# Optimization experiments

Measured on AMD Instinct MI355X. Metric: run time of the kernel, lower is better.

## Reference

```python
import jax, jax.numpy as jnp
import numpy as np

IM_SIZE = (256, 256)
OVERSAMP = 1.25
WIDTH = 6
BETA = float(np.pi * np.sqrt((WIDTH / OVERSAMP * (OVERSAMP - 0.5)) ** 2 - 0.8))
OS_SIZE = tuple(int(np.ceil(OVERSAMP * n)) for n in IM_SIZE)  # (320, 320)
D = 2


def _kb(x):
    # Kaiser-Bessel interpolation kernel: i0(beta*sqrt(1-x^2)) for |x|<=1 (sigpy convention)
    return jnp.i0(BETA * jnp.sqrt(jnp.maximum(1.0 - x * x, 0.0)))


def setup_inputs() -> dict:
    key = jax.random.key(0)
    k1, k2, k3 = jax.random.split(key, 3)
    N, C = 1, 8
    img_r = jax.random.normal(k1, (N, C) + IM_SIZE, dtype=jnp.float32)
    img_i = jax.random.normal(k2, (N, C) + IM_SIZE, dtype=jnp.float32)
    # trajectory in [-N_i/2, N_i/2] per the class docstring
    trj = (jax.random.uniform(k3, (N, 64, 4096, D), dtype=jnp.float32) - 0.5) * 256.0
    return {"img_r": img_r, "img_i": img_i, "trj": trj}


def _nufft_forward(img_r, img_i, trj):
    img = (img_r + 1j * img_i).astype(jnp.complex64)  # (N, C, H, W)
    nd = img.ndim
    # --- apodization (inverse FT of KB kernel), separable per axis ---
    for a in range(D):
        n, osn = IM_SIZE[a], OS_SIZE[a]
        idx = jnp.arange(n, dtype=jnp.float32)
        arg = jnp.sqrt(BETA ** 2 - (np.pi * WIDTH * (idx - n // 2) / osn) ** 2)
        apod = arg / jnp.sinh(arg)
        shape = [1] * nd
        shape[nd - D + a] = n
        img = img * apod.reshape(shape)
    # --- scale + centered zero-pad to oversampled grid ---
    img = img / np.sqrt(float(np.prod(IM_SIZE)))
    pads = [(0, 0)] * (nd - D) + [(((o - n) // 2), (o - n) - ((o - n) // 2))
                                  for n, o in zip(IM_SIZE, OS_SIZE)]
    img = jnp.pad(img, pads)
    # --- centered FFT (ifftshift -> fftn(norm=None) -> fftshift) ---
    axes = tuple(range(-D, 0))
    ksp_os = jnp.fft.fftshift(jnp.fft.fftn(jnp.fft.ifftshift(img, axes=axes), axes=axes), axes=axes)
    # --- scale trajectory to oversampled grid coordinates ---
    scale = jnp.array([OS_SIZE[a] / IM_SIZE[a] for a in range(D)], jnp.float32)
    shift = jnp.array([OS_SIZE[a] // 2 for a in range(D)], jnp.float32)
    coord = trj * scale + shift  # (N, R, S, 2)
    x0 = jnp.ceil(coord - WIDTH / 2.0)
    # --- KB interpolation: fixed 6x6 neighbor loop, vectorized gather over all points ---
    N = img.shape[0]
    out = jnp.zeros((N,) + img.shape[1:nd - D] + coord.shape[1:-1], jnp.complex64)

    def gather(grid, ix, iy):  # grid (C, Hos, Wos), ix/iy (R, S) -> (C, R, S)
        return grid[:, ix, iy]

    for dx in range(WIDTH):
        px = x0[..., 0] + dx
        wx = _kb((px - coord[..., 0]) / (WIDTH / 2.0))
        ix = px.astype(jnp.int32) % OS_SIZE[0]
        for dy in range(WIDTH):
            py = x0[..., 1] + dy
            wy = _kb((py - coord[..., 1]) / (WIDTH / 2.0))
            iy = py.astype(jnp.int32) % OS_SIZE[1]
            vals = jax.vmap(gather)(ksp_os, ix, iy)  # (N, C, R, S)
            out = out + vals * (wx * wy)[:, None, :, :]
    return out / (WIDTH ** D)


def reference(img_r, img_i, trj):
    return _nufft_forward(img_r, img_i, trj)
```

## Files before the change

### kernel.cpp

```cpp
#include <hip/hip_runtime.h>
#include <math.h>

#define NCH   8
#define IMN   256
#define OSN   320
#define NPTS  (64*4096)
#define KD    512
#define BETA_F   10.9551078f
#define BETA2_F  120.014389f
#define APOD_C   0.05890486225f

typedef unsigned short u16;
typedef unsigned int   u32;
typedef __attribute__((ext_vector_type(8))) short s16x8;
typedef __attribute__((ext_vector_type(4))) float f32x4;

__device__ __forceinline__ u32 f2bf(float f) {
    u32 u = __float_as_uint(f);
    return (u + 0x7FFFu + ((u >> 16) & 1u)) >> 16;
}

__device__ __forceinline__ float i0f(float t) {
    if (t < 3.75f) {
        float y = t * t * (1.0f / 14.0625f);
        return 1.0f + y * (3.5156229f + y * (3.0899424f + y * (1.2067492f +
                     y * (0.2659732f + y * (0.0360768f + y * 0.0045813f)))));
    }
    float z = 3.75f / t;
    float p = 0.39894228f + z * (0.01328592f + z * (0.00225319f + z * (-0.00157565f +
              z * (0.00916281f + z * (-0.02057706f + z * (0.02635537f +
              z * (-0.01647633f + z * 0.00392377f)))))));
    return expf(t) * rsqrtf(t) * p;
}

__device__ __forceinline__ float apodf(int i) {
    float x = APOD_C * (float)(i - IMN / 2);
    float arg = sqrtf(BETA2_F - x * x);
    float e = expf(arg);
    float sh = 0.5f * (e - 1.0f / e);
    return arg / sh;
}

__global__ void prep_const(u32* __restrict__ B1, u32* __restrict__ B2) {
    int idx = blockIdx.x * 256 + threadIdx.x;
    int k = idx >> 8, j = idx & 255;
    int p = (k * (j + 32)) % OSN;
    float th = (2.0f * (float)M_PI / (float)OSN) * (float)p;
    float s = ((k + j) & 1) ? -1.0f : 1.0f;
    float sn, cs;
    sincosf(th, &sn, &cs);
    float re = s * cs, im = -s * sn;
    B1[idx] = f2bf(re) | (f2bf(-im) << 16);
    B2[idx] = f2bf(im) | (f2bf(re) << 16);
}

__global__ void prep_a(const float* __restrict__ r, const float* __restrict__ im,
                       u32* __restrict__ A) {
    int idx = blockIdx.x * 256 + threadIdx.x;
    int i2 = idx & 255, i1 = (idx >> 8) & 255;
    float w = apodf(i1) * apodf(i2) * (1.0f / 256.0f);
    A[idx] = f2bf(r[idx] * w) | (f2bf(im[idx] * w) << 16);
}

__launch_bounds__(256)
__global__ void gemm1(const short* __restrict__ Abf, const short* __restrict__ B1,
                      const short* __restrict__ B2, short* __restrict__ Tb) {
    const int c = blockIdx.z;
    const int mBase = blockIdx.y * 64;
    const int nBase = blockIdx.x * 64;
    __shared__ short As[64][40], B1s[64][40], B2s[64][40];
    const int t = threadIdx.x;
    const int l = t & 63, w = t >> 6;
    const int wy = w >> 1, wx = w & 1;
    const int row = t >> 2, seg = (t & 3) * 8;
    const int fm = l & 15, fq = (l >> 4) * 8;
    f32x4 zz = {0.f, 0.f, 0.f, 0.f};
    f32x4 accRe[2][2], accIm[2][2];
    #pragma unroll
    for (int i = 0; i < 2; i++)
        #pragma unroll
        for (int j = 0; j < 2; j++) { accRe[i][j] = zz; accIm[i][j] = zz; }

    for (int kc = 0; kc < 16; kc++) {
        const int kb = kc * 32 + seg;
        *(s16x8*)&As [row][seg] = *(const s16x8*)(Abf + ((long)(c * IMN + mBase + row)) * KD + kb);
        *(s16x8*)&B1s[row][seg] = *(const s16x8*)(B1 + (long)(nBase + row) * KD + kb);
        *(s16x8*)&B2s[row][seg] = *(const s16x8*)(B2 + (long)(nBase + row) * KD + kb);
        __syncthreads();
        s16x8 a0  = *(const s16x8*)&As [wy * 32 + fm][fq];
        s16x8 a1  = *(const s16x8*)&As [wy * 32 + 16 + fm][fq];
        s16x8 b10 = *(const s16x8*)&B1s[wx * 32 + fm][fq];
        s16x8 b11 = *(const s16x8*)&B1s[wx * 32 + 16 + fm][fq];
        s16x8 b20 = *(const s16x8*)&B2s[wx * 32 + fm][fq];
        s16x8 b21 = *(const s16x8*)&B2s[wx * 32 + 16 + fm][fq];
        accRe[0][0] = __builtin_amdgcn_mfma_f32_16x16x32_bf16(a0, b10, accRe[0][0], 0, 0, 0);
        accRe[0][1] = __builtin_amdgcn_mfma_f32_16x16x32_bf16(a0, b11, accRe[0][1], 0, 0, 0);
        accRe[1][0] = __builtin_amdgcn_mfma_f32_16x16x32_bf16(a1, b10, accRe[1][0], 0, 0, 0);
        accRe[1][1] = __builtin_amdgcn_mfma_f32_16x16x32_bf16(a1, b11, accRe[1][1], 0, 0, 0);
        accIm[0][0] = __builtin_amdgcn_mfma_f32_16x16x32_bf16(a0, b20, accIm[0][0], 0, 0, 0);
        accIm[0][1] = __builtin_amdgcn_mfma_f32_16x16x32_bf16(a0, b21, accIm[0][1], 0, 0, 0);
        accIm[1][0] = __builtin_amdgcn_mfma_f32_16x16x32_bf16(a1, b20, accIm[1][0], 0, 0, 0);
        accIm[1][1] = __builtin_amdgcn_mfma_f32_16x16x32_bf16(a1, b21, accIm[1][1], 0, 0, 0);
        __syncthreads();
    }
    #pragma unroll
    for (int i = 0; i < 2; i++)
        #pragma unroll
        for (int j = 0; j < 2; j++) {
            int i1b = mBase + wy * 32 + i * 16 + (l >> 4) * 4;
            int k2  = nBase + wx * 32 + j * 16 + fm;
            s16x8 v;
            #pragma unroll
            for (int r = 0; r < 4; r++) {
                v[2 * r]     = (short)f2bf(accRe[i][j][r]);
                v[2 * r + 1] = (short)f2bf(accIm[i][j][r]);
            }
            *(s16x8*)(Tb + ((long)(c * OSN + k2)) * KD + 2 * i1b) = v;
        }
}

__launch_bounds__(256)
__global__ void gemm2(const short* __restrict__ B1, const short* __restrict__ B2,
                      const short* __restrict__ Tb, u32* __restrict__ Gb) {
    const int c = blockIdx.z;
    const int mBase = blockIdx.y * 64;
    const int nBase = blockIdx.x * 64;
    __shared__ short A1s[64][40], A2s[64][40], Bs[64][40];
    const int t = threadIdx.x;
    const int l = t & 63, w = t >> 6;
    const int wy = w >> 1, wx = w & 1;
    const int row = t >> 2, seg = (t & 3) * 8;
    const int fm = l & 15, fq = (l >> 4) * 8;
    f32x4 zz = {0.f, 0.f, 0.f, 0.f};
    f32x4 accRe[2][2], accIm[2][2];
    #pragma unroll
    for (int i = 0; i < 2; i++)
        #pragma unroll
        for (int j = 0; j < 2; j++) { accRe[i][j] = zz; accIm[i][j] = zz; }

    for (int kc = 0; kc < 16; kc++) {
        const int kb = kc * 32 + seg;
        *(s16x8*)&A1s[row][seg] = *(const s16x8*)(B1 + (long)(mBase + row) * KD + kb);
        *(s16x8*)&A2s[row][seg] = *(const s16x8*)(B2 + (long)(mBase + row) * KD + kb);
        *(s16x8*)&Bs [row][seg] = *(const s16x8*)(Tb + ((long)(c * OSN + nBase + row)) * KD + kb);
        __syncthreads();
        s16x8 a10 = *(const s16x8*)&A1s[wy * 32 + fm][fq];
        s16x8 a11 = *(const s16x8*)&A1s[wy * 32 + 16 + fm][fq];
        s16x8 a20 = *(const s16x8*)&A2s[wy * 32 + fm][fq];
        s16x8 a21 = *(const s16x8*)&A2s[wy * 32 + 16 + fm][fq];
        s16x8 b0  = *(const s16x8*)&Bs [wx * 32 + fm][fq];
        s16x8 b1  = *(const s16x8*)&Bs [wx * 32 + 16 + fm][fq];
        accRe[0][0] = __builtin_amdgcn_mfma_f32_16x16x32_bf16(a10, b0, accRe[0][0], 0, 0, 0);
        accRe[0][1] = __builtin_amdgcn_mfma_f32_16x16x32_bf16(a10, b1, accRe[0][1], 0, 0, 0);
        accRe[1][0] = __builtin_amdgcn_mfma_f32_16x16x32_bf16(a11, b0, accRe[1][0], 0, 0, 0);
        accRe[1][1] = __builtin_amdgcn_mfma_f32_16x16x32_bf16(a11, b1, accRe[1][1], 0, 0, 0);
        accIm[0][0] = __builtin_amdgcn_mfma_f32_16x16x32_bf16(a20, b0, accIm[0][0], 0, 0, 0);
        accIm[0][1] = __builtin_amdgcn_mfma_f32_16x16x32_bf16(a20, b1, accIm[0][1], 0, 0, 0);
        accIm[1][0] = __builtin_amdgcn_mfma_f32_16x16x32_bf16(a21, b0, accIm[1][0], 0, 0, 0);
        accIm[1][1] = __builtin_amdgcn_mfma_f32_16x16x32_bf16(a21, b1, accIm[1][1], 0, 0, 0);
        __syncthreads();
    }
    #pragma unroll
    for (int i = 0; i < 2; i++)
        #pragma unroll
        for (int j = 0; j < 2; j++) {
            int k2 = nBase + wx * 32 + j * 16 + fm;
            #pragma unroll
            for (int r = 0; r < 4; r++) {
                int k1 = mBase + wy * 32 + i * 16 + (l >> 4) * 4 + r;
                Gb[((long)k1 * OSN + k2) * NCH + c] =
                    f2bf(accRe[i][j][r]) | (f2bf(accIm[i][j][r]) << 16);
            }
        }
}

__global__ void interp_kernel(const float* __restrict__ trj,
                              const u32* __restrict__ grid,
                              u32* __restrict__ out) {
    const int t = threadIdx.x;
    const int c = t & 7;
    const int pl = t >> 3;
    __shared__ float wxs[32][6], wys[32][6];
    __shared__ int   x0s[32], y0s[32];

    if (t < 32) {
        int pt = blockIdx.x * 32 + t;
        float2 tv = *(const float2*)(trj + pt * 2);
        float cx = __fadd_rn(__fmul_rn(tv.x, 1.25f), 160.0f);
        float cy = __fadd_rn(__fmul_rn(tv.y, 1.25f), 160.0f);
        float x0 = ceilf(__fadd_rn(cx, -3.0f));
        float y0 = ceilf(__fadd_rn(cy, -3.0f));
        x0s[t] = (int)x0;
        y0s[t] = (int)y0;
        #pragma unroll
        for (int d = 0; d < 6; d++) {
            float u = __fdiv_rn(__fsub_rn(x0 + (float)d, cx), 3.0f);
            wxs[t][d] = i0f(BETA_F * sqrtf(fmaxf(1.0f - u * u, 0.0f)));
            float ww = __fdiv_rn(__fsub_rn(y0 + (float)d, cy), 3.0f);
            wys[t][d] = i0f(BETA_F * sqrtf(fmaxf(1.0f - ww * ww, 0.0f)));
        }
    }
    __syncthreads();

    int ix[6], iy[6];
    const int x0i = x0s[pl], y0i = y0s[pl];
    #pragma unroll
    for (int d = 0; d < 6; d++) {
        int vx = x0i + d;
        ix[d] = ((vx % OSN) + OSN) % OSN;
        int vy = y0i + d;
        iy[d] = ((vy % OSN) + OSN) % OSN;
    }

    float accRe = 0.f, accIm = 0.f;
    #pragma unroll
    for (int dx = 0; dx < 6; dx++) {
        long base = (long)ix[dx] * OSN;
        float wxv = wxs[pl][dx];
        #pragma unroll
        for (int dy = 0; dy < 6; dy++) {
            u32 g = grid[(base + iy[dy]) * NCH + c];
            float gre = __uint_as_float(g << 16);
            float gim = __uint_as_float(g & 0xFFFF0000u);
            float ww = wxv * wys[pl][dy];
            accRe += gre * ww;
            accIm += gim * ww;
        }
    }
    accRe *= (1.0f / 36.0f);
    accIm *= (1.0f / 36.0f);

    __shared__ float2 lds[256];
    lds[t] = make_float2(accRe, accIm);
    __syncthreads();
    int c2 = t >> 5, p2 = t & 31;
    float2 v = lds[p2 * 8 + c2];
    out[(long)c2 * NPTS + blockIdx.x * 32 + p2] = f2bf(v.y) | (f2bf(v.x) << 16);
}

extern "C" void kernel_launch(void* const* d_in, const int* in_sizes, int n_in,
                              void* d_out, int out_size, void* d_ws, size_t ws_size,
                              hipStream_t stream) {
    const float* img_r = (const float*)d_in[0];
    const float* img_i = (const float*)d_in[1];
    const float* trj   = (const float*)d_in[2];

    char* ob = (char*)d_out;
    short* Tb  = (short*)(ob);
    u32*  B1u  = (u32*)(ob + 2621440);
    u32*  B2u  = (u32*)(ob + 2949120);
    u32*  Au   = (u32*)(ob + 3276800);
    u32*  Gb   = (u32*)d_ws;

    prep_const<<<(OSN * IMN) / 256, 256, 0, stream>>>(B1u, B2u);
    prep_a<<<(NCH * IMN * IMN) / 256, 256, 0, stream>>>(img_r, img_i, Au);
    gemm1<<<dim3(OSN / 64, IMN / 64, NCH), 256, 0, stream>>>(
        (const short*)Au, (const short*)B1u, (const short*)B2u, Tb);
    gemm2<<<dim3(OSN / 64, OSN / 64, NCH), 256, 0, stream>>>(
        (const short*)B1u, (const short*)B2u, Tb, Gb);
    interp_kernel<<<NPTS / 32, 256, 0, stream>>>(trj, Gb, (u32*)d_out);
}
```

Before: 126.4 us.

## Halve GEMM tile width with 2-wave blocks and widen interp channel loads

Both DFT GEMMs now use 64x32 output tiles with 128-thread blocks, two waves each. This doubles the block count on the small per-channel grids so more CUs stay busy. The interpolation kernel now handles 64 points per block, and each thread loads two channels with one 8-byte load. That halves the gather instruction count and the trajectory/weight setup per point. The cost is lower per-block reuse of the shared B operand in the GEMMs and more register use in the interpolation.

```diff
diff --git a/kernel.cpp b/kernel.cpp
--- a/kernel.cpp
+++ b/kernel.cpp
@@ -62,17 +62,17 @@
     A[idx] = f2bf(r[idx] * w) | (f2bf(im[idx] * w) << 16);
 }
 
-__launch_bounds__(256)
+__launch_bounds__(128)
 __global__ void gemm1(const short* __restrict__ Abf, const short* __restrict__ B1,
                       const short* __restrict__ B2, short* __restrict__ Tb) {
     const int c = blockIdx.z;
     const int mBase = blockIdx.y * 64;
-    const int nBase = blockIdx.x * 64;
-    __shared__ short As[64][40], B1s[64][40], B2s[64][40];
+    const int nBase = blockIdx.x * 32;
+    __shared__ short As[64][40], B1s[32][40], B2s[32][40];
     const int t = threadIdx.x;
     const int l = t & 63, w = t >> 6;
-    const int wy = w >> 1, wx = w & 1;
-    const int row = t >> 2, seg = (t & 3) * 8;
+    const int arow = t >> 1, aseg = (t & 1) * 16;
+    const int brow = t >> 2, bseg = (t & 3) * 8;
     const int fm = l & 15, fq = (l >> 4) * 8;
     f32x4 zz = {0.f, 0.f, 0.f, 0.f};
     f32x4 accRe[2][2], accIm[2][2];
@@ -82,17 +82,21 @@
         for (int j = 0; j < 2; j++) { accRe[i][j] = zz; accIm[i][j] = zz; }
 
     for (int kc = 0; kc < 16; kc++) {
-        const int kb = kc * 32 + seg;
-        *(s16x8*)&As [row][seg] = *(const s16x8*)(Abf + ((long)(c * IMN + mBase + row)) * KD + kb);
-        *(s16x8*)&B1s[row][seg] = *(const s16x8*)(B1 + (long)(nBase + row) * KD + kb);
-        *(s16x8*)&B2s[row][seg] = *(const s16x8*)(B2 + (long)(nBase + row) * KD + kb);
-        __syncthreads();
-        s16x8 a0  = *(const s16x8*)&As [wy * 32 + fm][fq];
-        s16x8 a1  = *(const s16x8*)&As [wy * 32 + 16 + fm][fq];
-        s16x8 b10 = *(const s16x8*)&B1s[wx * 32 + fm][fq];
-        s16x8 b11 = *(const s16x8*)&B1s[wx * 32 + 16 + fm][fq];
-        s16x8 b20 = *(const s16x8*)&B2s[wx * 32 + fm][fq];
-        s16x8 b21 = *(const s16x8*)&B2s[wx * 32 + 16 + fm][fq];
+        const int kb = kc * 32;
+        {
+            const short* ap = Abf + ((long)(c * IMN + mBase + arow)) * KD + kb + aseg;
+            *(s16x8*)&As[arow][aseg]     = *(const s16x8*)(ap);
+            *(s16x8*)&As[arow][aseg + 8] = *(const s16x8*)(ap + 8);
+        }
+        *(s16x8*)&B1s[brow][bseg] = *(const s16x8*)(B1 + (long)(nBase + brow) * KD + kb + bseg);
+        *(s16x8*)&B2s[brow][bseg] = *(const s16x8*)(B2 + (long)(nBase + brow) * KD + kb + bseg);
+        __syncthreads();
+        s16x8 a0  = *(const s16x8*)&As [w * 32 + fm][fq];
+        s16x8 a1  = *(const s16x8*)&As [w * 32 + 16 + fm][fq];
+        s16x8 b10 = *(const s16x8*)&B1s[fm][fq];
+        s16x8 b11 = *(const s16x8*)&B1s[16 + fm][fq];
+        s16x8 b20 = *(const s16x8*)&B2s[fm][fq];
+        s16x8 b21 = *(const s16x8*)&B2s[16 + fm][fq];
         accRe[0][0] = __builtin_amdgcn_mfma_f32_16x16x32_bf16(a0, b10, accRe[0][0], 0, 0, 0);
         accRe[0][1] = __builtin_amdgcn_mfma_f32_16x16x32_bf16(a0, b11, accRe[0][1], 0, 0, 0);
         accRe[1][0] = __builtin_amdgcn_mfma_f32_16x16x32_bf16(a1, b10, accRe[1][0], 0, 0, 0);
@@ -107,8 +111,8 @@
     for (int i = 0; i < 2; i++)
         #pragma unroll
         for (int j = 0; j < 2; j++) {
-            int i1b = mBase + wy * 32 + i * 16 + (l >> 4) * 4;
-            int k2  = nBase + wx * 32 + j * 16 + fm;
+            int i1b = mBase + w * 32 + i * 16 + (l >> 4) * 4;
+            int k2  = nBase + j * 16 + fm;
             s16x8 v;
             #pragma unroll
             for (int r = 0; r < 4; r++) {
@@ -119,17 +123,17 @@
         }
 }
 
-__launch_bounds__(256)
+__launch_bounds__(128)
 __global__ void gemm2(const short* __restrict__ B1, const short* __restrict__ B2,
                       const short* __restrict__ Tb, u32* __restrict__ Gb) {
     const int c = blockIdx.z;
     const int mBase = blockIdx.y * 64;
-    const int nBase = blockIdx.x * 64;
-    __shared__ short A1s[64][40], A2s[64][40], Bs[64][40];
+    const int nBase = blockIdx.x * 32;
+    __shared__ short A1s[64][40], A2s[64][40], Bs[32][40];
     const int t = threadIdx.x;
     const int l = t & 63, w = t >> 6;
-    const int wy = w >> 1, wx = w & 1;
-    const int row = t >> 2, seg = (t & 3) * 8;
+    const int arow = t >> 1, aseg = (t & 1) * 16;
+    const int brow = t >> 2, bseg = (t & 3) * 8;
     const int fm = l & 15, fq = (l >> 4) * 8;
     f32x4 zz = {0.f, 0.f, 0.f, 0.f};
     f32x4 accRe[2][2], accIm[2][2];
@@ -139,17 +143,23 @@
         for (int j = 0; j < 2; j++) { accRe[i][j] = zz; accIm[i][j] = zz; }
 
     for (int kc = 0; kc < 16; kc++) {
-        const int kb = kc * 32 + seg;
-        *(s16x8*)&A1s[row][seg] = *(const s16x8*)(B1 + (long)(mBase + row) * KD + kb);
-        *(s16x8*)&A2s[row][seg] = *(const s16x8*)(B2 + (long)(mBase + row) * KD + kb);
-        *(s16x8*)&Bs [row][seg] = *(const s16x8*)(Tb + ((long)(c * OSN + nBase + row)) * KD + kb);
-        __syncthreads();
-        s16x8 a10 = *(const s16x8*)&A1s[wy * 32 + fm][fq];
-        s16x8 a11 = *(const s16x8*)&A1s[wy * 32 + 16 + fm][fq];
-        s16x8 a20 = *(const s16x8*)&A2s[wy * 32 + fm][fq];
-        s16x8 a21 = *(const s16x8*)&A2s[wy * 32 + 16 + fm][fq];
-        s16x8 b0  = *(const s16x8*)&Bs [wx * 32 + fm][fq];
-        s16x8 b1  = *(const s16x8*)&Bs [wx * 32 + 16 + fm][fq];
+        const int kb = kc * 32;
+        {
+            const short* a1p = B1 + (long)(mBase + arow) * KD + kb + aseg;
+            const short* a2p = B2 + (long)(mBase + arow) * KD + kb + aseg;
+            *(s16x8*)&A1s[arow][aseg]     = *(const s16x8*)(a1p);
+            *(s16x8*)&A1s[arow][aseg + 8] = *(const s16x8*)(a1p + 8);
+            *(s16x8*)&A2s[arow][aseg]     = *(const s16x8*)(a2p);
+            *(s16x8*)&A2s[arow][aseg + 8] = *(const s16x8*)(a2p + 8);
+        }
+        *(s16x8*)&Bs[brow][bseg] = *(const s16x8*)(Tb + ((long)(c * OSN + nBase + brow)) * KD + kb + bseg);
+        __syncthreads();
+        s16x8 a10 = *(const s16x8*)&A1s[w * 32 + fm][fq];
+        s16x8 a11 = *(const s16x8*)&A1s[w * 32 + 16 + fm][fq];
+        s16x8 a20 = *(const s16x8*)&A2s[w * 32 + fm][fq];
+        s16x8 a21 = *(const s16x8*)&A2s[w * 32 + 16 + fm][fq];
+        s16x8 b0  = *(const s16x8*)&Bs [fm][fq];
+        s16x8 b1  = *(const s16x8*)&Bs [16 + fm][fq];
         accRe[0][0] = __builtin_amdgcn_mfma_f32_16x16x32_bf16(a10, b0, accRe[0][0], 0, 0, 0);
         accRe[0][1] = __builtin_amdgcn_mfma_f32_16x16x32_bf16(a10, b1, accRe[0][1], 0, 0, 0);
         accRe[1][0] = __builtin_amdgcn_mfma_f32_16x16x32_bf16(a11, b0, accRe[1][0], 0, 0, 0);
@@ -164,10 +174,10 @@
     for (int i = 0; i < 2; i++)
         #pragma unroll
         for (int j = 0; j < 2; j++) {
-            int k2 = nBase + wx * 32 + j * 16 + fm;
+            int k2 = nBase + j * 16 + fm;
             #pragma unroll
             for (int r = 0; r < 4; r++) {
-                int k1 = mBase + wy * 32 + i * 16 + (l >> 4) * 4 + r;
+                int k1 = mBase + w * 32 + i * 16 + (l >> 4) * 4 + r;
                 Gb[((long)k1 * OSN + k2) * NCH + c] =
                     f2bf(accRe[i][j][r]) | (f2bf(accIm[i][j][r]) << 16);
             }
@@ -178,13 +188,13 @@
                               const u32* __restrict__ grid,
                               u32* __restrict__ out) {
     const int t = threadIdx.x;
-    const int c = t & 7;
-    const int pl = t >> 3;
-    __shared__ float wxs[32][6], wys[32][6];
-    __shared__ int   x0s[32], y0s[32];
-
-    if (t < 32) {
-        int pt = blockIdx.x * 32 + t;
+    const int pl = t >> 2;
+    const int cp = (t & 3) * 2;
+    __shared__ float wxs[64][6], wys[64][6];
+    __shared__ int   x0s[64], y0s[64];
+
+    if (t < 64) {
+        int pt = blockIdx.x * 64 + t;
         float2 tv = *(const float2*)(trj + pt * 2);
         float cx = __fadd_rn(__fmul_rn(tv.x, 1.25f), 160.0f);
         float cy = __fadd_rn(__fmul_rn(tv.y, 1.25f), 160.0f);
@@ -212,30 +222,34 @@
         iy[d] = ((vy % OSN) + OSN) % OSN;
     }
 
-    float accRe = 0.f, accIm = 0.f;
+    float re0 = 0.f, im0 = 0.f, re1 = 0.f, im1 = 0.f;
     #pragma unroll
     for (int dx = 0; dx < 6; dx++) {
         long base = (long)ix[dx] * OSN;
         float wxv = wxs[pl][dx];
         #pragma unroll
         for (int dy = 0; dy < 6; dy++) {
-            u32 g = grid[(base + iy[dy]) * NCH + c];
-            float gre = __uint_as_float(g << 16);
-            float gim = __uint_as_float(g & 0xFFFF0000u);
+            uint2 g = *(const uint2*)(grid + (base + iy[dy]) * NCH + cp);
             float ww = wxv * wys[pl][dy];
-            accRe += gre * ww;
-            accIm += gim * ww;
-        }
-    }
-    accRe *= (1.0f / 36.0f);
-    accIm *= (1.0f / 36.0f);
-
-    __shared__ float2 lds[256];
-    lds[t] = make_float2(accRe, accIm);
+            re0 += __uint_as_float(g.x << 16) * ww;
+            im0 += __uint_as_float(g.x & 0xFFFF0000u) * ww;
+            re1 += __uint_as_float(g.y << 16) * ww;
+            im1 += __uint_as_float(g.y & 0xFFFF0000u) * ww;
+        }
+    }
+    re0 *= (1.0f / 36.0f); im0 *= (1.0f / 36.0f);
+    re1 *= (1.0f / 36.0f); im1 *= (1.0f / 36.0f);
+
+    __shared__ float2 lds[64 * 8];
+    lds[pl * 8 + cp]     = make_float2(re0, im0);
+    lds[pl * 8 + cp + 1] = make_float2(re1, im1);
     __syncthreads();
     int c2 = t >> 5, p2 = t & 31;
-    float2 v = lds[p2 * 8 + c2];
-    out[(long)c2 * NPTS + blockIdx.x * 32 + p2] = f2bf(v.y) | (f2bf(v.x) << 16);
+    float2 va = lds[p2 * 8 + c2];
+    float2 vb = lds[(p2 + 32) * 8 + c2];
+    long ob = (long)c2 * NPTS + blockIdx.x * 64;
+    out[ob + p2]      = f2bf(va.y) | (f2bf(va.x) << 16);
+    out[ob + p2 + 32] = f2bf(vb.y) | (f2bf(vb.x) << 16);
 }
 
 extern "C" void kernel_launch(void* const* d_in, const int* in_sizes, int n_in,
@@ -254,9 +268,9 @@
 
     prep_const<<<(OSN * IMN) / 256, 256, 0, stream>>>(B1u, B2u);
     prep_a<<<(NCH * IMN * IMN) / 256, 256, 0, stream>>>(img_r, img_i, Au);
-    gemm1<<<dim3(OSN / 64, IMN / 64, NCH), 256, 0, stream>>>(
+    gemm1<<<dim3(OSN / 32, IMN / 64, NCH), 128, 0, stream>>>(
         (const short*)Au, (const short*)B1u, (const short*)B2u, Tb);
-    gemm2<<<dim3(OSN / 64, OSN / 64, NCH), 256, 0, stream>>>(
+    gemm2<<<dim3(OSN / 32, OSN / 64, NCH), 128, 0, stream>>>(
         (const short*)B1u, (const short*)B2u, Tb, Gb);
-    interp_kernel<<<NPTS / 32, 256, 0, stream>>>(trj, Gb, (u32*)d_out);
-}
+    interp_kernel<<<NPTS / 64, 256, 0, stream>>>(trj, Gb, (u32*)d_out);
+}
```

After: 116.5 us. -7.8%, faster.
